# Kernel optimization log

Measured on AMD Instinct MI355X. Metric: run time of the kernel, lower is better.

The kernel has to match this reference:

```python
import jax, jax.numpy as jnp
import numpy as np

B, T, HID = 2, 2048, 2048
NH, NKV, D = 16, 4, 128
WIN = 512
ROPE_BASE = 10000.0
SCALE = D ** -0.5
EPS = 1e-12


def setup_inputs() -> dict:
    key = jax.random.key(0)
    ks = jax.random.split(key, 5)
    x = jax.random.normal(ks[0], (B, T, HID), dtype=jnp.float32)
    wq = jax.random.normal(ks[1], (HID, NH * D), dtype=jnp.float32) * 0.02
    wk = jax.random.normal(ks[2], (HID, NKV * D), dtype=jnp.float32) * 0.02
    wv = jax.random.normal(ks[3], (HID, NKV * D), dtype=jnp.float32) * 0.02
    wo = jax.random.normal(ks[4], (NH * D, HID), dtype=jnp.float32) * 0.02
    return {"x": x, "wq": wq, "wk": wk, "wv": wv, "wo": wo}


def _rope_tables(t, offset=0):
    inv_freq = 1.0 / (ROPE_BASE ** (jnp.arange(0, D, 2, dtype=jnp.float32) / D))
    pos = jnp.arange(offset, offset + t, dtype=jnp.float32)
    freqs = pos[:, None] * inv_freq[None, :]              # [t, D/2]
    cos = jnp.concatenate([jnp.cos(freqs), jnp.cos(freqs)], axis=-1)  # [t, D]
    sin = jnp.concatenate([jnp.sin(freqs), jnp.sin(freqs)], axis=-1)
    return cos, sin


def _apply_rope(x, cos, sin):
    # x: [B, H, T, D]; rotate-half formulation
    x1, x2 = jnp.split(x, 2, axis=-1)
    rot = jnp.concatenate([-x2, x1], axis=-1)
    return x * cos[None, None] + rot * sin[None, None]


def _l2norm(x):
    n = jnp.sqrt(jnp.sum(x * x, axis=-1, keepdims=True))
    return x / jnp.maximum(n, EPS)


def _forward(x, wq, wk, wv, wo):
    b, t, _ = x.shape
    q = (x @ wq).reshape(b, t, NH, D).transpose(0, 2, 1, 3)    # [B,H,T,D]
    k = (x @ wk).reshape(b, t, NKV, D).transpose(0, 2, 1, 3)   # [B,Hk,T,D]
    v = (x @ wv).reshape(b, t, NKV, D).transpose(0, 2, 1, 3)
    q = _l2norm(q)
    k = _l2norm(k)
    cos, sin = _rope_tables(t, offset=0)
    q = _apply_rope(q, cos, sin)
    k = _apply_rope(k, cos, sin)
    rep = NH // NKV
    k = jnp.repeat(k, rep, axis=1)                             # GQA repeat_interleave
    v = jnp.repeat(v, rep, axis=1)
    i = jnp.arange(t)
    allowed = (i[None, :] <= i[:, None]) & (i[None, :] > i[:, None] - WIN)  # [T,T]
    logits = jnp.einsum("bhid,bhjd->bhij", q, k) * SCALE
    logits = jnp.where(allowed[None, None], logits, -jnp.inf)
    attn = jax.nn.softmax(logits, axis=-1)
    out = jnp.einsum("bhij,bhjd->bhid", attn, v)
    out = out.transpose(0, 2, 1, 3).reshape(b, t, NH * D)
    return out @ wo


def reference(x, wq, wk, wv, wo):
    return _forward(x, wq, wk, wv, wo)
```

## Files before the change

kernel.cpp:

```cpp
#include <hip/hip_runtime.h>
#include <hip/hip_bf16.h>
#include <cstdint>

#define NHQ 16
#define NKVH 4
#define HDIM 128
#define WINSZ 512
#define TSEQ 2048
#define ATTN_SCALE 0.08838834764831845f

typedef __attribute__((ext_vector_type(8))) short s16x8;
typedef __attribute__((ext_vector_type(4))) float f32x4;

__device__ __forceinline__ void gload16(const void* g, void* lds) {
  __builtin_amdgcn_global_load_lds(
      (const __attribute__((address_space(1))) unsigned int*)g,
      (__attribute__((address_space(3))) unsigned int*)(uintptr_t)lds,
      16, 0, 0);
}

__device__ __forceinline__ f32x4 mfma16(s16x8 a, s16x8 b, f32x4 c) {
  return __builtin_amdgcn_mfma_f32_16x16x32_bf16(a, b, c, 0, 0, 0);
}

#define SBAR() asm volatile("s_barrier" ::: "memory")
#define VMCNT(n) asm volatile("s_waitcnt vmcnt(" #n ")" ::: "memory")
#define LGKM(n) asm volatile("s_waitcnt lgkmcnt(" #n ")" ::: "memory")

__global__ __launch_bounds__(256) void rope_tables_kernel(float* __restrict__ cosT,
                                                          float* __restrict__ sinT) {
  int idx = blockIdx.x * 256 + threadIdx.x;
  int t = idx >> 6, d2 = idx & 63;
  float inv = powf(10000.0f, -(float)d2 / 64.0f);
  float a = (float)t * inv;
  cosT[idx] = cosf(a);
  sinT[idx] = sinf(a);
}

__global__ __launch_bounds__(256) void cast_kernel(const float* __restrict__ in,
                                                   __bf16* __restrict__ out, int n4) {
  int i = blockIdx.x * 256 + threadIdx.x;
  if (i >= n4) return;
  float4 v = ((const float4*)in)[i];
  union { __bf16 h[4]; uint2 u; } pk;
  pk.h[0] = (__bf16)v.x; pk.h[1] = (__bf16)v.y; pk.h[2] = (__bf16)v.z; pk.h[3] = (__bf16)v.w;
  ((uint2*)out)[i] = pk.u;
}

__global__ __launch_bounds__(256) void transpose_cast(const float* __restrict__ in,
                                                      __bf16* __restrict__ out, int R, int C) {
  __shared__ float tile[32][33];
  int c0 = blockIdx.x * 32, r0 = blockIdx.y * 32;
  int tx = threadIdx.x, ty = threadIdx.y;
#pragma unroll
  for (int i = 0; i < 4; i++)
    tile[ty + i * 8][tx] = in[(size_t)(r0 + ty + i * 8) * C + c0 + tx];
  __syncthreads();
#pragma unroll
  for (int i = 0; i < 4; i++)
    out[(size_t)(c0 + ty + i * 8) * R + r0 + tx] = (__bf16)tile[tx][ty + i * 8];
}

template <int MODE>
__global__ __launch_bounds__(512, 2) void gemm8(const __bf16* __restrict__ A,
                                                const __bf16* __restrict__ Bt,
                                                float* __restrict__ Cf,
                                                __bf16* __restrict__ Qo, __bf16* __restrict__ Ko,
                                                __bf16* __restrict__ Vo, int M, int N, int K) {
  __shared__ __attribute__((aligned(16))) char Lds[2][65536];

  const int tid = threadIdx.x;
  const int w = tid >> 6, lane = tid & 63;
  const int wm = w >> 2, wn = w & 3;

  const int nbx = gridDim.x;
  const int nwg = nbx * gridDim.y;
  const int bid = blockIdx.y * nbx + blockIdx.x;
  const int q8 = nwg >> 3, r8 = nwg & 7;
  const int xcd = bid & 7, idx = bid >> 3;
  const int swz = (xcd < r8 ? xcd * (q8 + 1) : r8 * (q8 + 1) + (xcd - r8) * q8) + idx;
  const int bx = swz % nbx, by = swz / nbx;
  const int m0 = by * 256, n0 = bx * 256;

  const int ru = tid >> 3;
  const int cs = (tid & 7) ^ (ru & 7);
  const __bf16* gAs = A + (size_t)(m0 + ru) * K + cs * 8;
  const __bf16* gBs = Bt + (size_t)(n0 + ru) * K + cs * 8;

  auto stA = [&](int tt, int u) {
    gload16(gAs + (size_t)(64 * u) * K + tt * 64, Lds[tt & 1] + u * 8192 + w * 1024);
  };
  auto stB = [&](int tt, int u) {
    gload16(gBs + (size_t)(64 * u) * K + tt * 64, Lds[tt & 1] + 32768 + u * 8192 + w * 1024);
  };

  const int rowb = (lane & 15) * 128;
  const int cph0 = (((lane >> 4)) ^ (lane & 7)) * 16;
  const int cph1 = ((4 + (lane >> 4)) ^ (lane & 7)) * 16;
  const int Abase = wm * 16384;
  const int Bbase = 32768 + wn * 8192;

  f32x4 acc[8][4];
  f32x4 zero = {0.f, 0.f, 0.f, 0.f};
#pragma unroll
  for (int i = 0; i < 8; i++)
#pragma unroll
    for (int j = 0; j < 4; j++) acc[i][j] = zero;

  const int NT = K >> 6;

#pragma unroll
  for (int u = 0; u < 4; u++) stA(0, u);
#pragma unroll
  for (int u = 0; u < 4; u++) stB(0, u);
#pragma unroll
  for (int u = 0; u < 4; u++) stA(1, u);
#pragma unroll
  for (int u = 0; u < 4; u++) stB(1, u);
  VMCNT(8);
  SBAR();

  s16x8 fa[4][2], fb[4][2];

  for (int t = 0; t < NT; ++t) {
    const char* bs = Lds[t & 1];
    const bool more = (t + 2) < NT;

#pragma unroll
    for (int mi = 0; mi < 4; mi++) {
      fa[mi][0] = *(const s16x8*)(bs + Abase + mi * 2048 + rowb + cph0);
      fa[mi][1] = *(const s16x8*)(bs + Abase + mi * 2048 + rowb + cph1);
    }
#pragma unroll
    for (int ni = 0; ni < 2; ni++) {
      fb[ni][0] = *(const s16x8*)(bs + Bbase + ni * 2048 + rowb + cph0);
      fb[ni][1] = *(const s16x8*)(bs + Bbase + ni * 2048 + rowb + cph1);
    }
    SBAR();
    LGKM(0);
    __builtin_amdgcn_sched_barrier(0);
    __builtin_amdgcn_s_setprio(1);
#pragma unroll
    for (int mi = 0; mi < 4; mi++)
#pragma unroll
      for (int ni = 0; ni < 2; ni++)
#pragma unroll
        for (int kk = 0; kk < 2; kk++)
          acc[mi][ni] = mfma16(fa[mi][kk], fb[ni][kk], acc[mi][ni]);
    __builtin_amdgcn_s_setprio(0);
    SBAR();

#pragma unroll
    for (int ni = 2; ni < 4; ni++) {
      fb[ni][0] = *(const s16x8*)(bs + Bbase + ni * 2048 + rowb + cph0);
      fb[ni][1] = *(const s16x8*)(bs + Bbase + ni * 2048 + rowb + cph1);
    }
    if (more) { stA(t + 2, 0); stA(t + 2, 2); }
    SBAR();
    LGKM(0);
    __builtin_amdgcn_sched_barrier(0);
    __builtin_amdgcn_s_setprio(1);
#pragma unroll
    for (int mi = 0; mi < 4; mi++)
#pragma unroll
      for (int ni = 2; ni < 4; ni++)
#pragma unroll
        for (int kk = 0; kk < 2; kk++)
          acc[mi][ni] = mfma16(fa[mi][kk], fb[ni][kk], acc[mi][ni]);
    __builtin_amdgcn_s_setprio(0);
    SBAR();

#pragma unroll
    for (int mi = 0; mi < 4; mi++) {
      fa[mi][0] = *(const s16x8*)(bs + Abase + 8192 + mi * 2048 + rowb + cph0);
      fa[mi][1] = *(const s16x8*)(bs + Abase + 8192 + mi * 2048 + rowb + cph1);
    }
    if (more) { stB(t + 2, 0); stB(t + 2, 1); stB(t + 2, 2); stB(t + 2, 3); }
    SBAR();
    LGKM(0);
    __builtin_amdgcn_sched_barrier(0);
    __builtin_amdgcn_s_setprio(1);
#pragma unroll
    for (int mi = 0; mi < 4; mi++)
#pragma unroll
      for (int ni = 0; ni < 2; ni++)
#pragma unroll
        for (int kk = 0; kk < 2; kk++)
          acc[4 + mi][ni] = mfma16(fa[mi][kk], fb[ni][kk], acc[4 + mi][ni]);
    __builtin_amdgcn_s_setprio(0);
    SBAR();

    if (more) { stA(t + 2, 1); stA(t + 2, 3); }
    if (t + 2 < NT) {
      VMCNT(8);
    } else if (t + 1 < NT) {
      VMCNT(0);
    }
    SBAR();
    __builtin_amdgcn_s_setprio(1);
#pragma unroll
    for (int mi = 0; mi < 4; mi++)
#pragma unroll
      for (int ni = 2; ni < 4; ni++)
#pragma unroll
        for (int kk = 0; kk < 2; kk++)
          acc[4 + mi][ni] = mfma16(fa[mi][kk], fb[ni][kk], acc[4 + mi][ni]);
    __builtin_amdgcn_s_setprio(0);
    SBAR();
  }

#pragma unroll
  for (int mf = 0; mf < 8; mf++)
#pragma unroll
    for (int nf = 0; nf < 4; nf++) {
      int rbase = m0 + wm * 128 + mf * 16 + (lane >> 4) * 4;
      int col = n0 + wn * 64 + nf * 16 + (lane & 15);
#pragma unroll
      for (int r = 0; r < 4; r++) {
        int m = rbase + r;
        float v = acc[mf][nf][r];
        if constexpr (MODE == 0) {
          Cf[(size_t)m * N + col] = v;
        } else {
          int b = m >> 11, tq = m & 2047;
          __bf16 bv = (__bf16)v;
          if (col < 2048) {
            Qo[(((size_t)(b * NHQ + (col >> 7))) * TSEQ + tq) * HDIM + (col & 127)] = bv;
          } else if (col < 2560) {
            int c2 = col - 2048;
            Ko[(((size_t)(b * NKVH + (c2 >> 7))) * TSEQ + tq) * HDIM + (c2 & 127)] = bv;
          } else {
            int c2 = col - 2560;
            Vo[(((size_t)(b * NKVH + (c2 >> 7))) * TSEQ + tq) * HDIM + (c2 & 127)] = bv;
          }
        }
      }
    }
}

__global__ __launch_bounds__(256) void normrope(__bf16* __restrict__ Q, __bf16* __restrict__ Kk,
                                                const float* __restrict__ cosT,
                                                const float* __restrict__ sinT) {
  int w = threadIdx.x >> 6, lane = threadIdx.x & 63;
  int row = blockIdx.x / 5;
  int slot = (blockIdx.x % 5) * 4 + w;
  int b = row >> 11, t = row & 2047;
  __bf16* p;
  if (slot < 16)
    p = Q + (((size_t)(b * NHQ + slot)) * TSEQ + t) * HDIM;
  else
    p = Kk + (((size_t)(b * NKVH + (slot - 16))) * TSEQ + t) * HDIM;
  float x1 = (float)p[lane], x2 = (float)p[lane + 64];
  float ss = x1 * x1 + x2 * x2;
#pragma unroll
  for (int off = 32; off; off >>= 1) ss += __shfl_xor(ss, off);
  float inv = 1.0f / fmaxf(sqrtf(ss), 1e-12f);
  x1 *= inv;
  x2 *= inv;
  float c = cosT[t * 64 + lane], s = sinT[t * 64 + lane];
  p[lane] = (__bf16)(x1 * c - x2 * s);
  p[lane + 64] = (__bf16)(x2 * c + x1 * s);
}

__global__ __launch_bounds__(512, 4) void attn_kernel(const __bf16* __restrict__ Qf,
                                                      const __bf16* __restrict__ Kf,
                                                      const __bf16* __restrict__ Vf,
                                                      __bf16* __restrict__ Ab) {
  __shared__ __attribute__((aligned(16))) char KlB[64 * 256];
  __shared__ __attribute__((aligned(16))) char VtB[128 * 128];
  __shared__ __attribute__((aligned(16))) char PlB[8 * 2048];
  int tid = threadIdx.x, w = tid >> 6, lane = tid & 63;
  int bid = blockIdx.x;
  int qt = bid & 15, bh = bid >> 4;
  int b = bh >> 4, h = bh & 15;
  int qs = qt * 128;
  int kvh = h >> 2;
  const __bf16* Qb = Qf + ((size_t)(b * NHQ + h) * TSEQ) * HDIM;
  const __bf16* Kb = Kf + ((size_t)(b * NKVH + kvh) * TSEQ) * HDIM;
  const __bf16* Vb = Vf + ((size_t)(b * NKVH + kvh) * TSEQ) * HDIM;
  char* Pw = PlB + w * 2048;

  s16x8 aq[4];
  int qrow_f = qs + w * 16 + (lane & 15);
#pragma unroll
  for (int kb = 0; kb < 4; kb++)
    aq[kb] = *(const s16x8*)(Qb + (size_t)qrow_f * HDIM + kb * 32 + (lane >> 4) * 8);

  f32x4 acc[8];
  f32x4 zero = {0.f, 0.f, 0.f, 0.f};
#pragma unroll
  for (int db = 0; db < 8; db++) acc[db] = zero;
  float mrow[4], lrow[4];
#pragma unroll
  for (int r = 0; r < 4; r++) { mrow[r] = -1e30f; lrow[r] = 0.f; }

  int lo = qs - (WINSZ - 1);
  if (lo < 0) lo = 0;
  lo &= ~63;
  const int nt = ((qs + 128) - lo) >> 6;

  const int kjr = tid >> 3, kkc = tid & 7;
  const int vk = tid & 63, vg = tid >> 6;

  int4 kR[2], vR[2];

#define ATTN_LOAD(KS)                                                              \
  _Pragma("unroll") for (int i = 0; i < 2; i++) {                                  \
    kR[i] = *(const int4*)(Kb + (size_t)((KS) + kjr) * HDIM + (kkc + 8 * i) * 8);  \
    vR[i] = *(const int4*)(Vb + (size_t)((KS) + vk) * HDIM + (vg + 8 * i) * 8);    \
  }

#define ATTN_WRITE()                                                               \
  _Pragma("unroll") for (int i = 0; i < 2; i++) {                                  \
    *(int4*)(KlB + kjr * 256 + (((kkc + 8 * i) * 16) ^ ((kjr & 7) << 4))) = kR[i]; \
    const __bf16* pv = (const __bf16*)&vR[i];                                      \
    int d0 = (vg + 8 * i) * 8;                                                     \
    _Pragma("unroll") for (int e = 0; e < 8; e++) {                                \
      int d = d0 + e;                                                              \
      *(__bf16*)(VtB + d * 128 + ((vk * 2) ^ ((d & 7) << 4))) = pv[e];             \
    }                                                                              \
  }

#define ATTN_COMPUTE(KS)                                                           \
  {                                                                                \
    f32x4 sacc[4];                                                                 \
    _Pragma("unroll") for (int jb = 0; jb < 4; jb++) sacc[jb] = zero;              \
    __builtin_amdgcn_s_setprio(1);                                                 \
    _Pragma("unroll") for (int jb = 0; jb < 4; jb++) {                             \
      int key = jb * 16 + (lane & 15);                                             \
      _Pragma("unroll") for (int kb = 0; kb < 4; kb++) {                           \
        s16x8 bk = *(const s16x8*)(KlB + key * 256 +                               \
                                   ((kb * 64 + (lane >> 4) * 16) ^ ((key & 7) << 4))); \
        sacc[jb] = mfma16(aq[kb], bk, sacc[jb]);                                   \
      }                                                                            \
    }                                                                              \
    __builtin_amdgcn_s_setprio(0);                                                 \
    float scf[4];                                                                  \
    _Pragma("unroll") for (int r = 0; r < 4; r++) {                                \
      int qrow = qs + w * 16 + (lane >> 4) * 4 + r;                                \
      float sv[4]; bool av[4];                                                     \
      _Pragma("unroll") for (int jb = 0; jb < 4; jb++) {                           \
        int j = (KS) + jb * 16 + (lane & 15);                                      \
        av[jb] = (j <= qrow) && (j > qrow - WINSZ);                                \
        sv[jb] = sacc[jb][r] * ATTN_SCALE;                                         \
      }                                                                            \
      float mt = -1e30f;                                                           \
      _Pragma("unroll") for (int jb = 0; jb < 4; jb++)                             \
        mt = fmaxf(mt, av[jb] ? sv[jb] : -1e30f);                                  \
      _Pragma("unroll") for (int off = 1; off < 16; off <<= 1)                     \
        mt = fmaxf(mt, __shfl_xor(mt, off));                                       \
      float mn = fmaxf(mrow[r], mt);                                               \
      float pv_[4]; float ts = 0.f;                                                \
      _Pragma("unroll") for (int jb = 0; jb < 4; jb++) {                           \
        pv_[jb] = av[jb] ? __expf(sv[jb] - mn) : 0.f;                              \
        ts += pv_[jb];                                                             \
      }                                                                            \
      _Pragma("unroll") for (int off = 1; off < 16; off <<= 1)                     \
        ts += __shfl_xor(ts, off);                                                 \
      float sf = __expf(mrow[r] - mn);                                             \
      lrow[r] = lrow[r] * sf + ts;                                                 \
      mrow[r] = mn;                                                                \
      scf[r] = sf;                                                                 \
      int q = (lane >> 4) * 4 + r;                                                 \
      _Pragma("unroll") for (int jb = 0; jb < 4; jb++)                             \
        *(__bf16*)(Pw + q * 128 +                                                  \
                   (((jb * 16 + (lane & 15)) * 2) ^ ((q & 7) << 4))) = (__bf16)pv_[jb]; \
    }                                                                              \
    s16x8 pa[2];                                                                   \
    _Pragma("unroll") for (int kb = 0; kb < 2; kb++) {                             \
      int q = lane & 15;                                                           \
      pa[kb] = *(const s16x8*)(Pw + q * 128 +                                      \
                               ((kb * 64 + (lane >> 4) * 16) ^ ((q & 7) << 4)));   \
    }                                                                              \
    _Pragma("unroll") for (int db = 0; db < 8; db++) {                             \
      f32x4 tt = acc[db];                                                          \
      _Pragma("unroll") for (int r = 0; r < 4; r++) tt[r] *= scf[r];               \
      acc[db] = tt;                                                                \
    }                                                                              \
    __builtin_amdgcn_s_setprio(1);                                                 \
    _Pragma("unroll") for (int db = 0; db < 8; db++) {                             \
      int d = db * 16 + (lane & 15);                                               \
      _Pragma("unroll") for (int kb = 0; kb < 2; kb++) {                           \
        s16x8 bv = *(const s16x8*)(VtB + d * 128 +                                 \
                                   ((kb * 64 + (lane >> 4) * 16) ^ ((d & 7) << 4))); \
        acc[db] = mfma16(pa[kb], bv, acc[db]);                                     \
      }                                                                            \
    }                                                                              \
    __builtin_amdgcn_s_setprio(0);                                                 \
  }

  ATTN_LOAD(lo);
  ATTN_WRITE();
  __syncthreads();

  int ks = lo;
  for (int t = 0; t < nt; ++t) {
    if (t + 1 < nt) ATTN_LOAD(ks + 64);
    int qmin = qs + w * 16, qmax = qmin + 15;
    if (ks <= qmax && ks + 63 > qmin - WINSZ) ATTN_COMPUTE(ks);
    __syncthreads();
    if (t + 1 < nt) {
      ATTN_WRITE();
      __syncthreads();
    }
    ks += 64;
  }

#undef ATTN_LOAD
#undef ATTN_WRITE
#undef ATTN_COMPUTE

#pragma unroll
  for (int db = 0; db < 8; db++)
#pragma unroll
    for (int r = 0; r < 4; r++) {
      int qrow = qs + w * 16 + (lane >> 4) * 4 + r;
      float v = acc[db][r] / lrow[r];
      Ab[((size_t)(b * TSEQ + qrow)) * 2048 + h * HDIM + db * 16 + (lane & 15)] = (__bf16)v;
    }
}

extern "C" void kernel_launch(void* const* d_in, const int* in_sizes, int n_in,
                              void* d_out, int out_size, void* d_ws, size_t ws_size,
                              hipStream_t stream) {
  const float* x = (const float*)d_in[0];
  const float* wq = (const float*)d_in[1];
  const float* wk = (const float*)d_in[2];
  const float* wv = (const float*)d_in[3];
  const float* wo = (const float*)d_in[4];
  float* out = (float*)d_out;

  char* ws = (char*)d_ws;
  size_t off = 0;
  auto alloc = [&](size_t bytes) -> void* {
    void* p = ws + off;
    off += (bytes + 255) & ~(size_t)255;
    return p;
  };
  __bf16* Xb = (__bf16*)alloc((size_t)4096 * 2048 * 2);
  __bf16* Wqkvt = (__bf16*)alloc((size_t)3072 * 2048 * 2);
  __bf16* Wot = (__bf16*)alloc((size_t)2048 * 2048 * 2);
  __bf16* Q = (__bf16*)alloc((size_t)2 * NHQ * TSEQ * HDIM * 2);
  __bf16* Kb = (__bf16*)alloc((size_t)2 * NKVH * TSEQ * HDIM * 2);
  __bf16* Vb = (__bf16*)alloc((size_t)2 * NKVH * TSEQ * HDIM * 2);
  float* cosT = (float*)alloc((size_t)TSEQ * 64 * 4);
  float* sinT = (float*)alloc((size_t)TSEQ * 64 * 4);
  __bf16* Ab = Xb;

  rope_tables_kernel<<<TSEQ * 64 / 256, 256, 0, stream>>>(cosT, sinT);
  cast_kernel<<<8192, 256, 0, stream>>>(x, Xb, 2097152);
  dim3 tb(32, 8);
  transpose_cast<<<dim3(64, 64), tb, 0, stream>>>(wq, Wqkvt, 2048, 2048);
  transpose_cast<<<dim3(16, 64), tb, 0, stream>>>(wk, Wqkvt + (size_t)2048 * 2048, 2048, 512);
  transpose_cast<<<dim3(16, 64), tb, 0, stream>>>(wv, Wqkvt + (size_t)2560 * 2048, 2048, 512);
  transpose_cast<<<dim3(64, 64), tb, 0, stream>>>(wo, Wot, 2048, 2048);

  gemm8<1><<<dim3(12, 16), 512, 0, stream>>>(Xb, Wqkvt, nullptr, Q, Kb, Vb, 4096, 3072, 2048);
  normrope<<<4096 * 5, 256, 0, stream>>>(Q, Kb, cosT, sinT);
  attn_kernel<<<2 * NHQ * (TSEQ / 128), 512, 0, stream>>>(Q, Kb, Vb, Ab);
  gemm8<0><<<dim3(8, 16), 512, 0, stream>>>(Ab, Wot, out, nullptr, nullptr, nullptr, 4096, 2048,
                                            2048);
}
```

Measured before the change: 263.0 us.

## Drop online softmax max tracking using L2-normed bounded logits, shrink attention tiles

New measurement: 233.3 us. -11.3%, faster.

```diff
diff --git a/kernel.cpp b/kernel.cpp
--- a/kernel.cpp
+++ b/kernel.cpp
@@ -255,6 +255,7 @@
 #pragma unroll
   for (int off = 32; off; off >>= 1) ss += __shfl_xor(ss, off);
   float inv = 1.0f / fmaxf(sqrtf(ss), 1e-12f);
+  if (slot < 16) inv *= ATTN_SCALE;
   x1 *= inv;
   x2 *= inv;
   float c = cosT[t * 64 + lane], s = sinT[t * 64 + lane];
@@ -262,18 +263,18 @@
   p[lane + 64] = (__bf16)(x2 * c + x1 * s);
 }
 
-__global__ __launch_bounds__(512, 4) void attn_kernel(const __bf16* __restrict__ Qf,
-                                                      const __bf16* __restrict__ Kf,
-                                                      const __bf16* __restrict__ Vf,
-                                                      __bf16* __restrict__ Ab) {
+__global__ __launch_bounds__(256) void attn_kernel(const __bf16* __restrict__ Qf,
+                                                   const __bf16* __restrict__ Kf,
+                                                   const __bf16* __restrict__ Vf,
+                                                   __bf16* __restrict__ Ab) {
   __shared__ __attribute__((aligned(16))) char KlB[64 * 256];
   __shared__ __attribute__((aligned(16))) char VtB[128 * 128];
-  __shared__ __attribute__((aligned(16))) char PlB[8 * 2048];
+  __shared__ __attribute__((aligned(16))) char PlB[4 * 2048];
   int tid = threadIdx.x, w = tid >> 6, lane = tid & 63;
   int bid = blockIdx.x;
-  int qt = bid & 15, bh = bid >> 4;
-  int b = bh >> 4, h = bh & 15;
-  int qs = qt * 128;
+  int qt = (bid + 7 * (bid >> 5)) & 31;
+  int h = (bid >> 5) & 15, b = bid >> 9;
+  int qs = qt * 64;
   int kvh = h >> 2;
   const __bf16* Qb = Qf + ((size_t)(b * NHQ + h) * TSEQ) * HDIM;
   const __bf16* Kb = Kf + ((size_t)(b * NKVH + kvh) * TSEQ) * HDIM;
@@ -290,31 +291,32 @@
   f32x4 zero = {0.f, 0.f, 0.f, 0.f};
 #pragma unroll
   for (int db = 0; db < 8; db++) acc[db] = zero;
-  float mrow[4], lrow[4];
-#pragma unroll
-  for (int r = 0; r < 4; r++) { mrow[r] = -1e30f; lrow[r] = 0.f; }
+  float lsum[4];
+#pragma unroll
+  for (int r = 0; r < 4; r++) lsum[r] = 0.f;
 
   int lo = qs - (WINSZ - 1);
   if (lo < 0) lo = 0;
   lo &= ~63;
-  const int nt = ((qs + 128) - lo) >> 6;
-
-  const int kjr = tid >> 3, kkc = tid & 7;
+  const int nt = ((qs + 64) - lo) >> 6;
+
+  const int kjr = tid >> 4, kkc = tid & 15;
   const int vk = tid & 63, vg = tid >> 6;
 
-  int4 kR[2], vR[2];
+  int4 kR[4], vR[4];
 
 #define ATTN_LOAD(KS)                                                              \
-  _Pragma("unroll") for (int i = 0; i < 2; i++) {                                  \
-    kR[i] = *(const int4*)(Kb + (size_t)((KS) + kjr) * HDIM + (kkc + 8 * i) * 8);  \
-    vR[i] = *(const int4*)(Vb + (size_t)((KS) + vk) * HDIM + (vg + 8 * i) * 8);    \
+  _Pragma("unroll") for (int i = 0; i < 4; i++) {                                  \
+    kR[i] = *(const int4*)(Kb + (size_t)((KS) + kjr + 16 * i) * HDIM + kkc * 8);   \
+    vR[i] = *(const int4*)(Vb + (size_t)((KS) + vk) * HDIM + (vg + 4 * i) * 8);    \
   }
 
 #define ATTN_WRITE()                                                               \
-  _Pragma("unroll") for (int i = 0; i < 2; i++) {                                  \
-    *(int4*)(KlB + kjr * 256 + (((kkc + 8 * i) * 16) ^ ((kjr & 7) << 4))) = kR[i]; \
+  _Pragma("unroll") for (int i = 0; i < 4; i++) {                                  \
+    int jr = kjr + 16 * i;                                                         \
+    *(int4*)(KlB + jr * 256 + ((kkc * 16) ^ ((jr & 7) << 4))) = kR[i];             \
     const __bf16* pv = (const __bf16*)&vR[i];                                      \
-    int d0 = (vg + 8 * i) * 8;                                                     \
+    int d0 = (vg + 4 * i) * 8;                                                     \
     _Pragma("unroll") for (int e = 0; e < 8; e++) {                                \
       int d = d0 + e;                                                              \
       *(__bf16*)(VtB + d * 128 + ((vk * 2) ^ ((d & 7) << 4))) = pv[e];             \
@@ -335,47 +337,25 @@
       }                                                                            \
     }                                                                              \
     __builtin_amdgcn_s_setprio(0);                                                 \
-    float scf[4];                                                                  \
     _Pragma("unroll") for (int r = 0; r < 4; r++) {                                \
       int qrow = qs + w * 16 + (lane >> 4) * 4 + r;                                \
-      float sv[4]; bool av[4];                                                     \
+      int q = (lane >> 4) * 4 + r;                                                 \
+      float ps = 0.f;                                                              \
       _Pragma("unroll") for (int jb = 0; jb < 4; jb++) {                           \
         int j = (KS) + jb * 16 + (lane & 15);                                      \
-        av[jb] = (j <= qrow) && (j > qrow - WINSZ);                                \
-        sv[jb] = sacc[jb][r] * ATTN_SCALE;                                         \
+        bool av = (j <= qrow) && (j > qrow - WINSZ);                               \
+        float pv_ = av ? __expf(sacc[jb][r]) : 0.f;                                \
+        ps += pv_;                                                                 \
+        *(__bf16*)(Pw + q * 128 +                                                  \
+                   (((jb * 16 + (lane & 15)) * 2) ^ ((q & 7) << 4))) = (__bf16)pv_; \
       }                                                                            \
-      float mt = -1e30f;                                                           \
-      _Pragma("unroll") for (int jb = 0; jb < 4; jb++)                             \
-        mt = fmaxf(mt, av[jb] ? sv[jb] : -1e30f);                                  \
-      _Pragma("unroll") for (int off = 1; off < 16; off <<= 1)                     \
-        mt = fmaxf(mt, __shfl_xor(mt, off));                                       \
-      float mn = fmaxf(mrow[r], mt);                                               \
-      float pv_[4]; float ts = 0.f;                                                \
-      _Pragma("unroll") for (int jb = 0; jb < 4; jb++) {                           \
-        pv_[jb] = av[jb] ? __expf(sv[jb] - mn) : 0.f;                              \
-        ts += pv_[jb];                                                             \
-      }                                                                            \
-      _Pragma("unroll") for (int off = 1; off < 16; off <<= 1)                     \
-        ts += __shfl_xor(ts, off);                                                 \
-      float sf = __expf(mrow[r] - mn);                                             \
-      lrow[r] = lrow[r] * sf + ts;                                                 \
-      mrow[r] = mn;                                                                \
-      scf[r] = sf;                                                                 \
-      int q = (lane >> 4) * 4 + r;                                                 \
-      _Pragma("unroll") for (int jb = 0; jb < 4; jb++)                             \
-        *(__bf16*)(Pw + q * 128 +                                                  \
-                   (((jb * 16 + (lane & 15)) * 2) ^ ((q & 7) << 4))) = (__bf16)pv_[jb]; \
+      lsum[r] += ps;                                                               \
     }                                                                              \
     s16x8 pa[2];                                                                   \
     _Pragma("unroll") for (int kb = 0; kb < 2; kb++) {                             \
       int q = lane & 15;                                                           \
       pa[kb] = *(const s16x8*)(Pw + q * 128 +                                      \
                                ((kb * 64 + (lane >> 4) * 16) ^ ((q & 7) << 4)));   \
-    }                                                                              \
-    _Pragma("unroll") for (int db = 0; db < 8; db++) {                             \
-      f32x4 tt = acc[db];                                                          \
-      _Pragma("unroll") for (int r = 0; r < 4; r++) tt[r] *= scf[r];               \
-      acc[db] = tt;                                                                \
     }                                                                              \
     __builtin_amdgcn_s_setprio(1);                                                 \
     _Pragma("unroll") for (int db = 0; db < 8; db++) {                             \
@@ -396,8 +376,7 @@
   int ks = lo;
   for (int t = 0; t < nt; ++t) {
     if (t + 1 < nt) ATTN_LOAD(ks + 64);
-    int qmin = qs + w * 16, qmax = qmin + 15;
-    if (ks <= qmax && ks + 63 > qmin - WINSZ) ATTN_COMPUTE(ks);
+    ATTN_COMPUTE(ks);
     __syncthreads();
     if (t + 1 < nt) {
       ATTN_WRITE();
@@ -411,11 +390,17 @@
 #undef ATTN_COMPUTE
 
 #pragma unroll
+  for (int r = 0; r < 4; r++) {
+#pragma unroll
+    for (int off = 1; off < 16; off <<= 1) lsum[r] += __shfl_xor(lsum[r], off);
+    lsum[r] = 1.0f / lsum[r];
+  }
+#pragma unroll
   for (int db = 0; db < 8; db++)
 #pragma unroll
     for (int r = 0; r < 4; r++) {
       int qrow = qs + w * 16 + (lane >> 4) * 4 + r;
-      float v = acc[db][r] / lrow[r];
+      float v = acc[db][r] * lsum[r];
       Ab[((size_t)(b * TSEQ + qrow)) * 2048 + h * HDIM + db * 16 + (lane & 15)] = (__bf16)v;
     }
 }
@@ -457,7 +442,7 @@
 
   gemm8<1><<<dim3(12, 16), 512, 0, stream>>>(Xb, Wqkvt, nullptr, Q, Kb, Vb, 4096, 3072, 2048);
   normrope<<<4096 * 5, 256, 0, stream>>>(Q, Kb, cosT, sinT);
-  attn_kernel<<<2 * NHQ * (TSEQ / 128), 512, 0, stream>>>(Q, Kb, Vb, Ab);
+  attn_kernel<<<2 * NHQ * (TSEQ / 64), 256, 0, stream>>>(Q, Kb, Vb, Ab);
   gemm8<0><<<dim3(8, 16), 512, 0, stream>>>(Ab, Wot, out, nullptr, nullptr, nullptr, 4096, 2048,
                                             2048);
 }
```
